# Performance work log

Hardware: AMD Instinct MI355X
Metric: run time of the kernel (lower is better)

## Reference

```python
import jax, jax.numpy as jnp
import numpy as np

DILATIONS = [1, 2, 4, 8, 16, 32, 64, 128, 256, 512] * 2
WD = 128   # residual/gate channels
SD = 512   # skip channels
VOCAB = 256
FIELD = int(np.sum(DILATIONS)) + 2  # receptive field = 2048


def setup_inputs() -> dict:
    key = jax.random.key(0)
    ks = jax.random.split(key, 10)
    B, T = 4, 16384
    L = len(DILATIONS)
    y = jax.random.randint(ks[0], (B, T), 0, VOCAB)
    embed = jax.random.normal(ks[1], (VOCAB, WD), dtype=jnp.float32) * 0.1
    # dilated causal conv: kernel_size=2, wd -> 2*wd (gate stacking)
    Wd = jax.random.normal(ks[2], (L, 2 * WD, WD, 2), dtype=jnp.float32) * 0.05
    bd = jnp.zeros((L, 2 * WD), dtype=jnp.float32)
    # skip 1x1 conv: wd -> sd
    Ws = jax.random.normal(ks[3], (L, SD, WD, 1), dtype=jnp.float32) * 0.05
    bs = jnp.zeros((L, SD), dtype=jnp.float32)
    # residual 1x1 conv: wd -> wd
    Wr = jax.random.normal(ks[4], (L, WD, WD, 1), dtype=jnp.float32) * 0.05
    br = jnp.zeros((L, WD), dtype=jnp.float32)
    # post convs (bias=False)
    W1 = jax.random.normal(ks[5], (SD, SD, 1), dtype=jnp.float32) * 0.05
    W2 = jax.random.normal(ks[6], (VOCAB, SD, 1), dtype=jnp.float32) * 0.05
    return {"y": y, "embed": embed, "Wd": Wd, "bd": bd, "Ws": Ws,
            "bs": bs, "Wr": Wr, "br": br, "W1": W1, "W2": W2}


def reference(y, embed, Wd, bd, Ws, bs, Wr, br, W1, W2):
    # embedding -> [B, C, T]
    x = jnp.transpose(embed[y], (0, 2, 1))
    finalout = x.shape[2] - (FIELD - 1)
    skip = None
    for i, d in enumerate(DILATIONS):
        # dilated valid conv with kernel size 2 == two shifted 1x1 matmuls
        in_act = (jnp.einsum('oc,bct->bot', Wd[i, :, :, 0], x[:, :, :-d]) +
                  jnp.einsum('oc,bct->bot', Wd[i, :, :, 1], x[:, :, d:]) +
                  bd[i][None, :, None])                       # [B, 2*WD, T-d]
        acts = jnp.tanh(in_act[:, :WD]) * jax.nn.sigmoid(in_act[:, WD:])
        res = jnp.einsum('oc,bct->bot', Wr[i, :, :, 0], acts) + br[i][None, :, None]
        sk = (jnp.einsum('oc,bct->bot', Ws[i, :, :, 0], acts[:, :, -finalout:]) +
              bs[i][None, :, None])                            # [B, SD, finalout]
        skip = sk if skip is None else skip + sk
        x = res + x[:, :, d:]
    out = jax.nn.relu(skip)
    out = jax.nn.relu(jnp.einsum('oc,bct->bot', W1[:, :, 0], out))
    out = jnp.einsum('oc,bct->bot', W2[:, :, 0], out)          # [B, 256, finalout]
    return out
```

## Files before the change

### kernel.cpp

```cpp
#include <hip/hip_runtime.h>
#include <cstddef>

#define B_    4
#define T_    16384
#define FOUT_ 14337
#define FOUTP 14464
#define NL_   20
#define XSTR  ((size_t)T_*128)
#define ABSTR ((size_t)FOUTP*128)
#define ALSTR ((size_t)B_*FOUTP*128)
#define SBSTR ((size_t)FOUTP*512)

typedef float    f32x16 __attribute__((ext_vector_type(16)));
typedef _Float16 f16x8  __attribute__((ext_vector_type(8)));

__device__ _Float16 g_xh0[(size_t)B_*T_*128];
__device__ _Float16 g_xh1[(size_t)B_*T_*128];
__device__ _Float16 g_WdF0[(size_t)NL_*256*128];
__device__ _Float16 g_WdF1[(size_t)NL_*256*128];
__device__ _Float16 g_WrF [(size_t)NL_*128*128];
__device__ _Float16 g_WsF [(size_t)512*2560];
__device__ _Float16 g_W1F [(size_t)512*512];
__device__ _Float16 g_W2F [(size_t)256*512];
__device__ float    g_bssum[512];
__device__ _Float16 g_acts[(size_t)NL_*B_*FOUTP*128];
__device__ _Float16 g_skipF[(size_t)B_*FOUTP*512];
__device__ _Float16 g_h1F [(size_t)B_*FOUTP*512];

__device__ __forceinline__ float sigm_(float x){ return 1.0f/(1.0f+__expf(-x)); }
__device__ __forceinline__ float tanh_(float x){ return 1.0f - 2.0f/(__expf(2.0f*x)+1.0f); }
__device__ __forceinline__ f32x16 MFMA32(f16x8 a, f16x8 b, f32x16 c){
  return __builtin_amdgcn_mfma_f32_32x32x16_f16(a, b, c, 0, 0, 0);
}

typedef const __attribute__((address_space(1))) _Float16 gash;
typedef __attribute__((address_space(3))) _Float16 lash;
__device__ __forceinline__ void gld_lds16(const _Float16* g, _Float16* l){
  __builtin_amdgcn_global_load_lds((gash*)g, (lash*)l, 16, 0, 0);
}

__global__ void cvt_wd(const float* __restrict__ Wd){
  int i = blockIdx.x*256 + threadIdx.x;
  if (i >= NL_*256*16) return;
  int row = i >> 4, koct = i & 15;
  const float* s = Wd + ((size_t)row*128 + koct*8)*2;
  int lane = (koct&1)*32 + (row&31);
  size_t addr = (size_t)((row>>5)*8 + (koct>>1))*512 + lane*8;
  union { _Float16 h[8]; uint4 v; } u0, u1;
#pragma unroll
  for (int j=0;j<8;j++){ u0.h[j]=(_Float16)s[2*j]; u1.h[j]=(_Float16)s[2*j+1]; }
  *(uint4*)((void*)(g_WdF0 + addr)) = u0.v;
  *(uint4*)((void*)(g_WdF1 + addr)) = u1.v;
}
__global__ void cvt_rm(const float* __restrict__ src, int which, int M, int K){
  int i = blockIdx.x*256 + threadIdx.x;
  if (i >= M*(K>>3)) return;
  int row = i / (K>>3), koct = i % (K>>3);
  const float* s = src + (size_t)row*K + koct*8;
  int lane = (koct&1)*32 + (row&31);
  size_t addr = ((size_t)(row>>5)*(K>>4) + (koct>>1))*512 + lane*8;
  union { _Float16 h[8]; uint4 v; } u;
#pragma unroll
  for (int j=0;j<8;j++) u.h[j]=(_Float16)s[j];
  _Float16* dst = (which==0)?g_WrF:(which==1)?g_W1F:g_W2F;
  *(uint4*)((void*)(dst + addr)) = u.v;
}
__global__ void cvt_ws(const float* __restrict__ Ws){
  int i = blockIdx.x*256 + threadIdx.x;
  if (i >= NL_*512*16) return;
  int l = i >> 13, o = (i>>4)&511, coct = i&15;
  const float* s = Ws + ((size_t)(l*512+o))*128 + coct*8;
  int lane = (coct&1)*32 + (o&31);
  size_t addr = ((size_t)(o>>5)*160 + (size_t)(l*8 + (coct>>1)))*512 + lane*8;
  union { _Float16 h[8]; uint4 v; } u;
#pragma unroll
  for (int j=0;j<8;j++) u.h[j]=(_Float16)s[j];
  *(uint4*)((void*)(g_WsF + addr)) = u.v;
}
__global__ void bssum_k(const float* __restrict__ bs){
  int o = threadIdx.x;
  float s = 0.f;
  for (int l=0;l<NL_;l++) s += bs[l*512 + o];
  g_bssum[o] = s;
}

__global__ void embed_kernel(const int* __restrict__ y, const float* __restrict__ embed){
  int gid = blockIdx.x*256 + threadIdx.x;
  int bt = gid >> 4, c8 = gid & 15;
  if (bt < B_*T_){
    int idx = y[bt];
    const float* e = embed + (size_t)idx*128 + c8*8;
    union { _Float16 h[8]; uint4 v; } u;
#pragma unroll
    for (int j=0;j<8;j++) u.h[j]=(_Float16)e[j];
    *(uint4*)((void*)(g_xh0 + (size_t)bt*128 + c8*8)) = u.v;
  }
}

__global__ __launch_bounds__(256,3) void layer16(
    int swap, int l, int d, int Tout, int ss,
    const float* __restrict__ bd_l, const float* __restrict__ br_l)
{
  const _Float16* __restrict__ xin  = swap ? g_xh1 : g_xh0;
  _Float16* __restrict__       xout = swap ? g_xh0 : g_xh1;

  __shared__ _Float16 X0s[16*520];
  __shared__ _Float16 X1s[16*520];
  __shared__ _Float16 ACs[16*520];

  const int tid = threadIdx.x;
  const int w   = tid >> 6;
  const int lane= tid & 63;
  const int ln2 = lane & 31;
  const int h   = lane >> 5;
  const int b   = blockIdx.y;
  const int t0  = blockIdx.x*64;
  const int ntv = min(64, Tout - t0);
  const int limit = Tout + d - 1;
  const _Float16* __restrict__ xb = xin + (size_t)b*XSTR;

#pragma unroll
  for (int it=0; it<4; it++){
    int t = (tid>>4) + it*16, c16 = tid&15;
    int s0 = t0 + t;     if (s0 > limit) s0 = limit;
    int s1 = t0 + t + d; if (s1 > limit) s1 = limit;
    *(uint4*)((void*)&X0s[c16*520 + t*8]) = *(const uint4*)((const void*)(xb + (size_t)s0*128 + c16*8));
    *(uint4*)((void*)&X1s[c16*520 + t*8]) = *(const uint4*)((const void*)(xb + (size_t)s1*128 + c16*8));
  }
  __syncthreads();

  f32x16 aB[2][2];
#pragma unroll
  for (int mi=0;mi<2;mi++)
#pragma unroll
    for (int nt=0;nt<2;nt++)
#pragma unroll
      for (int r=0;r<16;r++) aB[mi][nt][r] = 0.f;

#pragma unroll
  for (int tap=0; tap<2; tap++){
    const _Float16* __restrict__ Xs = tap ? X1s : X0s;
    const _Float16* __restrict__ Wt = (tap ? g_WdF1 : g_WdF0) + (size_t)l*32768;
    const _Float16* aT = Wt + (size_t)w*4096 + lane*8;
    const _Float16* aS = Wt + (size_t)(4+w)*4096 + lane*8;
#pragma unroll
    for (int ks=0; ks<8; ks++){
      f16x8 bfr[2];
#pragma unroll
      for (int nt=0; nt<2; nt++)
        bfr[nt] = *(const f16x8*)((const void*)&Xs[(ks*2+h)*520 + (nt*32+ln2)*8]);
      f16x8 fT = *(const f16x8*)((const void*)(aT + ks*512));
      f16x8 fS = *(const f16x8*)((const void*)(aS + ks*512));
#pragma unroll
      for (int nt=0; nt<2; nt++){
        aB[0][nt] = MFMA32(fT, bfr[nt], aB[0][nt]);
        aB[1][nt] = MFMA32(fS, bfr[nt], aB[1][nt]);
      }
    }
  }

#pragma unroll
  for (int nt=0; nt<2; nt++)
#pragma unroll
    for (int rq=0; rq<4; rq++){
      int c0 = w*32 + rq*8 + 4*h;
      union { _Float16 hh[4]; ushort4 v; } pk;
#pragma unroll
      for (int rr=0; rr<4; rr++){
        float it_ = aB[0][nt][rq*4+rr] + bd_l[c0+rr];
        float is_ = aB[1][nt][rq*4+rr] + bd_l[128+c0+rr];
        pk.hh[rr] = (_Float16)(tanh_(it_)*sigm_(is_));
      }
      *(ushort4*)((void*)&ACs[(w*4+rq)*520 + (nt*32+ln2)*8 + 4*h]) = pk.v;
    }
  __syncthreads();

  f32x16 aC[2];
#pragma unroll
  for (int nt=0;nt<2;nt++)
#pragma unroll
    for (int r=0;r<16;r++) aC[nt][r] = 0.f;
  {
    const _Float16* aW = g_WrF + (size_t)l*16384 + (size_t)w*4096 + lane*8;
#pragma unroll
    for (int ks=0; ks<8; ks++){
      f16x8 bfr[2];
#pragma unroll
      for (int nt=0; nt<2; nt++)
        bfr[nt] = *(const f16x8*)((const void*)&ACs[(ks*2+h)*520 + (nt*32+ln2)*8]);
      f16x8 fW = *(const f16x8*)((const void*)(aW + ks*512));
#pragma unroll
      for (int nt=0; nt<2; nt++)
        aC[nt] = MFMA32(fW, bfr[nt], aC[nt]);
    }
  }

#pragma unroll
  for (int nt=0; nt<2; nt++){
    int t = nt*32 + ln2;
    if (t < ntv){
      size_t xrow = (size_t)b*XSTR + (size_t)(t0+t)*128;
#pragma unroll
      for (int rq=0; rq<4; rq++){
        int c0 = w*32 + rq*8 + 4*h;
        union { ushort4 v; _Float16 hh[4]; } xr;
        xr.v = *(const ushort4*)((const void*)&X1s[(w*4+rq)*520 + t*8 + 4*h]);
        union { _Float16 hh[4]; ushort4 v; } ov;
#pragma unroll
        for (int rr=0; rr<4; rr++)
          ov.hh[rr] = (_Float16)(aC[nt][rq*4+rr] + br_l[c0+rr] + (float)xr.hh[rr]);
        *(ushort4*)((void*)(xout + xrow + c0)) = ov.v;
      }
    }
  }

  _Float16* __restrict__ actsB = g_acts + (size_t)l*ALSTR + (size_t)b*ABSTR;
#pragma unroll
  for (int it=0; it<4; it++){
    int t = (tid>>4) + it*16, c16 = tid&15;
    int ts = t0 + t - ss;
    if (t < ntv && ts >= 0 && ts < FOUT_){
      size_t addr = (size_t)(ts>>5)*4096 + (size_t)(c16>>1)*512 + ((c16&1)*32 + (ts&31))*8;
      *(uint4*)((void*)(actsB + addr)) = *(const uint4*)((const void*)&ACs[c16*520 + t*8]);
    }
  }
}

template<int MODE>
__global__ __launch_bounds__(512,2) void gemm_stream(float* __restrict__ outF){
  constexpr int NSTEP = (MODE==0)?160:32;
  constexpr int NCH   = NSTEP/8;
  constexpr int MFR   = (MODE==2)?1:2;
  const _Float16* __restrict__ A    = (MODE==0)?g_WsF:(MODE==1)?g_W1F:g_W2F;
  const _Float16* __restrict__ Bsrc = (MODE==0)?g_acts:(MODE==1)?g_skipF:g_h1F;

  __shared__ __align__(16) _Float16 Bs[2][16384];

  const int tid = threadIdx.x;
  const int w   = tid >> 6;
  const int lane= tid & 63;
  const int ln2 = lane & 31;
  const int h   = lane >> 5;
  const int b   = blockIdx.y;
  const int ts0 = blockIdx.x*128;

  const _Float16* Gb[4];
#pragma unroll
  for (int nt=0;nt<4;nt++){
    size_t tile = blockIdx.x*4 + nt;
    Gb[nt] = (MODE==0) ? (Bsrc + (size_t)b*ABSTR + tile*4096  + lane*8)
                       : (Bsrc + (size_t)b*SBSTR + tile*16384 + lane*8);
  }
  const size_t cstr = (MODE==0) ? (size_t)ALSTR : (size_t)4096;

  const _Float16* Ab[MFR];
#pragma unroll
  for (int mi=0;mi<MFR;mi++)
    Ab[mi] = A + (size_t)(w*MFR+mi)*((size_t)NSTEP*512) + lane*8;

  f32x16 acc[MFR][4];
#pragma unroll
  for (int mi=0;mi<MFR;mi++)
#pragma unroll
    for (int nt=0;nt<4;nt++)
#pragma unroll
      for (int r=0;r<16;r++) acc[mi][nt][r] = 0.f;

  auto STAGE = [&](int buf, int c){
#pragma unroll
    for (int nt=0;nt<4;nt++){
      const _Float16* g = Gb[nt] + (size_t)c*cstr + (size_t)w*512;
      gld_lds16(g, &Bs[buf][((size_t)(w*4+nt))*512]);
    }
  };

  auto COMPUTE = [&](int buf, int c){
#pragma unroll
    for (int ks=0; ks<8; ks++){
      f16x8 bfr[4];
#pragma unroll
      for (int nt=0;nt<4;nt++)
        bfr[nt] = *(const f16x8*)((const void*)&Bs[buf][(size_t)(ks*4+nt)*512 + lane*8]);
      f16x8 af[MFR];
#pragma unroll
      for (int mi=0;mi<MFR;mi++)
        af[mi] = *(const f16x8*)((const void*)(Ab[mi] + ((size_t)c*8 + ks)*512));
#pragma unroll
      for (int mi=0;mi<MFR;mi++)
#pragma unroll
        for (int nt=0;nt<4;nt++)
          acc[mi][nt] = MFMA32(af[mi], bfr[nt], acc[mi][nt]);
    }
  };

  STAGE(0, 0);
  asm volatile("s_waitcnt vmcnt(0)" ::: "memory");
  __syncthreads();
  int cur = 0;
  for (int c=0; c<NCH; ++c){
    if (c+1 < NCH) STAGE(cur^1, c+1);
    COMPUTE(cur, c);
    __syncthreads();
    cur ^= 1;
  }

  if (MODE != 2){
    _Float16* __restrict__ dstb = ((MODE==0)?g_skipF:g_h1F) + (size_t)b*SBSTR;
#pragma unroll
    for (int mi=0; mi<MFR; mi++){
      int mtile = w*MFR+mi;
#pragma unroll
      for (int nt=0; nt<4; nt++){
        int ts = ts0 + nt*32 + ln2;
        if (ts >= FOUT_) continue;
#pragma unroll
        for (int rq=0; rq<4; rq++){
          int m0 = mtile*32 + rq*8 + 4*h;
          union { _Float16 hh[4]; ushort4 v; } pk;
#pragma unroll
          for (int rr=0; rr<4; rr++){
            float vv = acc[mi][nt][rq*4+rr];
            if (MODE==0) vv += g_bssum[m0+rr];
            pk.hh[rr] = (_Float16)fmaxf(vv, 0.f);
          }
          size_t addr = (size_t)(ts>>5)*16384 + (size_t)(mtile*2 + (rq>>1))*512
                      + ((rq&1)*32 + (ts&31))*8 + 4*h;
          *(ushort4*)((void*)(dstb + addr)) = pk.v;
        }
      }
    }
  } else {
#pragma unroll
    for (int nt=0; nt<4; nt++){
      int ts = ts0 + nt*32 + ln2;
      if (ts >= FOUT_) continue;
#pragma unroll
      for (int rq=0; rq<4; rq++){
        int m0 = w*32 + rq*8 + 4*h;
#pragma unroll
        for (int rr=0; rr<4; rr++)
          outF[((size_t)(b*256 + m0 + rr))*FOUT_ + ts] = acc[0][nt][rq*4+rr];
      }
    }
  }
}

extern "C" void kernel_launch(void* const* d_in, const int* in_sizes, int n_in,
                              void* d_out, int out_size, void* d_ws, size_t ws_size,
                              hipStream_t stream) {
  const int*   y     = (const int*)  d_in[0];
  const float* embed = (const float*)d_in[1];
  const float* Wd    = (const float*)d_in[2];
  const float* bd    = (const float*)d_in[3];
  const float* Ws    = (const float*)d_in[4];
  const float* bs    = (const float*)d_in[5];
  const float* Wr    = (const float*)d_in[6];
  const float* br    = (const float*)d_in[7];
  const float* W1    = (const float*)d_in[8];
  const float* W2    = (const float*)d_in[9];
  float* out = (float*)d_out;
  (void)d_ws; (void)ws_size;

  cvt_wd<<<dim3(320), dim3(256), 0, stream>>>(Wd);
  cvt_rm<<<dim3(160), dim3(256), 0, stream>>>(Wr, 0, NL_*128, 128);
  cvt_rm<<<dim3(128), dim3(256), 0, stream>>>(W1, 1, 512, 512);
  cvt_rm<<<dim3( 64), dim3(256), 0, stream>>>(W2, 2, 256, 512);
  cvt_ws<<<dim3(640), dim3(256), 0, stream>>>(Ws);
  bssum_k<<<dim3(1), dim3(512), 0, stream>>>(bs);

  embed_kernel<<<dim3((B_*T_*16)/256), dim3(256), 0, stream>>>(y, embed);

  static const int DIL[NL_] = {1,2,4,8,16,32,64,128,256,512,
                               1,2,4,8,16,32,64,128,256,512};
  int swap = 0;
  int Tin = T_;
  for (int i=0;i<NL_;i++){
    int d = DIL[i];
    int Tout = Tin - d;
    dim3 grid((Tout+63)/64, B_);
    layer16<<<grid, dim3(256), 0, stream>>>(
        swap, i, d, Tout, Tout - FOUT_, bd + (size_t)i*256, br + (size_t)i*128);
    swap ^= 1;
    Tin = Tout;
  }

  dim3 gg(FOUTP/128, B_);
  gemm_stream<0><<<gg, dim3(512), 0, stream>>>(nullptr);
  gemm_stream<1><<<gg, dim3(512), 0, stream>>>(nullptr);
  gemm_stream<2><<<gg, dim3(512), 0, stream>>>(out);
}
```

Measured before the change: 972.5 us.

## Restructure streaming GEMM into four-buffer ring with prefetch distance two

Replaces the double-buffered 8-kstep chunk loop in gemm_stream with a 4-slot LDS ring of 4-kstep sub-chunks, prefetched two steps ahead. The A fragments for a sub-chunk are loaded up front, and sched_barriers pin the order of loads, the next stage and the MFMAs. The aim is to hide global-to-LDS latency behind more in-flight stages without a full vmcnt(0) drain each iteration. In exchange there are twice as many block barriers, and correctness depends on implicit vmcnt ordering between the A loads and the stage loads.

```diff
diff --git a/kernel.cpp b/kernel.cpp
--- a/kernel.cpp
+++ b/kernel.cpp
@@ -229,12 +229,12 @@
 template<int MODE>
 __global__ __launch_bounds__(512,2) void gemm_stream(float* __restrict__ outF){
   constexpr int NSTEP = (MODE==0)?160:32;
-  constexpr int NCH   = NSTEP/8;
+  constexpr int NSC   = NSTEP/4;
   constexpr int MFR   = (MODE==2)?1:2;
   const _Float16* __restrict__ A    = (MODE==0)?g_WsF:(MODE==1)?g_W1F:g_W2F;
   const _Float16* __restrict__ Bsrc = (MODE==0)?g_acts:(MODE==1)?g_skipF:g_h1F;
 
-  __shared__ __align__(16) _Float16 Bs[2][16384];
+  __shared__ __align__(16) _Float16 Bs[4][8192];
 
   const int tid = threadIdx.x;
   const int w   = tid >> 6;
@@ -251,7 +251,10 @@
     Gb[nt] = (MODE==0) ? (Bsrc + (size_t)b*ABSTR + tile*4096  + lane*8)
                        : (Bsrc + (size_t)b*SBSTR + tile*16384 + lane*8);
   }
-  const size_t cstr = (MODE==0) ? (size_t)ALSTR : (size_t)4096;
+  auto baddr = [&](int nt, int ks) -> const _Float16* {
+    return (MODE==0) ? (Gb[nt] + (size_t)(ks>>3)*ALSTR + (size_t)(ks&7)*512)
+                     : (Gb[nt] + (size_t)ks*512);
+  };
 
   const _Float16* Ab[MFR];
 #pragma unroll
@@ -266,42 +269,46 @@
 #pragma unroll
       for (int r=0;r<16;r++) acc[mi][nt][r] = 0.f;
 
-  auto STAGE = [&](int buf, int c){
-#pragma unroll
-    for (int nt=0;nt<4;nt++){
-      const _Float16* g = Gb[nt] + (size_t)c*cstr + (size_t)w*512;
-      gld_lds16(g, &Bs[buf][((size_t)(w*4+nt))*512]);
+  auto STAGE = [&](int buf, int sc){
+#pragma unroll
+    for (int q=0;q<2;q++){
+      int bi  = w*2 + q;
+      int ksl = bi>>2, nt = bi&3;
+      gld_lds16(baddr(nt, sc*4+ksl), &Bs[buf][(size_t)bi*512]);
     }
   };
 
-  auto COMPUTE = [&](int buf, int c){
-#pragma unroll
-    for (int ks=0; ks<8; ks++){
+  STAGE(0,0);
+  STAGE(1,1);
+  asm volatile("s_waitcnt vmcnt(2)" ::: "memory");
+  __builtin_amdgcn_sched_barrier(0);
+  __builtin_amdgcn_s_barrier();
+
+  for (int c=0; c<NSC; ++c){
+    const int buf = c & 3;
+    f16x8 af[MFR][4];
+#pragma unroll
+    for (int mi=0;mi<MFR;mi++)
+#pragma unroll
+      for (int j=0;j<4;j++)
+        af[mi][j] = *(const f16x8*)((const void*)(Ab[mi] + (size_t)(c*4+j)*512));
+    __builtin_amdgcn_sched_barrier(0);
+    if (c+2 < NSC) STAGE((c+2)&3, c+2);
+    __builtin_amdgcn_sched_barrier(0);
+#pragma unroll
+    for (int j=0;j<4;j++){
       f16x8 bfr[4];
 #pragma unroll
       for (int nt=0;nt<4;nt++)
-        bfr[nt] = *(const f16x8*)((const void*)&Bs[buf][(size_t)(ks*4+nt)*512 + lane*8]);
-      f16x8 af[MFR];
+        bfr[nt] = *(const f16x8*)((const void*)&Bs[buf][(size_t)(j*4+nt)*512 + lane*8]);
 #pragma unroll
       for (int mi=0;mi<MFR;mi++)
-        af[mi] = *(const f16x8*)((const void*)(Ab[mi] + ((size_t)c*8 + ks)*512));
-#pragma unroll
-      for (int mi=0;mi<MFR;mi++)
 #pragma unroll
         for (int nt=0;nt<4;nt++)
-          acc[mi][nt] = MFMA32(af[mi], bfr[nt], acc[mi][nt]);
-    }
-  };
-
-  STAGE(0, 0);
-  asm volatile("s_waitcnt vmcnt(0)" ::: "memory");
-  __syncthreads();
-  int cur = 0;
-  for (int c=0; c<NCH; ++c){
-    if (c+1 < NCH) STAGE(cur^1, c+1);
-    COMPUTE(cur, c);
-    __syncthreads();
-    cur ^= 1;
+          acc[mi][nt] = MFMA32(af[mi][j], bfr[nt], acc[mi][nt]);
+    }
+    __builtin_amdgcn_sched_barrier(0);
+    __builtin_amdgcn_s_barrier();
   }
 
   if (MODE != 2){
```

New measurement: 959.6 us. No clear change (-1.3%).
